# Performance work log

Measured on AMD Instinct MI355X. Metric: run time of the kernel, lower is better.

The kernel has to match this reference:

```python
import jax, jax.numpy as jnp
import numpy as np

# hyperparams matching init_kwargs
T_LEN = 1024
T_LATENCY = 7
TB = T_LATENCY + 1          # t_len_block
N_OUT = 1024
BATCH = 32
FS_SCALE = 10.0             # FastSigmoid default scale


@jax.custom_vjp
def fast_sigmoid(x):
    # forward: Heaviside; backward: fast-sigmoid surrogate
    return (x > 0).astype(x.dtype)

def _fs_fwd(x):
    return (x > 0).astype(x.dtype), x

def _fs_bwd(x, g):
    return (g / (FS_SCALE * jnp.abs(x) + 1.0) ** 2,)

fast_sigmoid.defvjp(_fs_fwd, _fs_bwd)


def setup_inputs() -> dict:
    key = jax.random.key(0)
    k1, k2, k3, k4 = jax.random.split(key, 4)
    x = jax.random.normal(k1, (T_LEN, BATCH, N_OUT), dtype=jnp.float32) * 0.6
    # raw params; forward applies the clamp/abs 'properties' of the module
    beta_raw = jax.random.uniform(k2, (N_OUT,), minval=0.7, maxval=0.99, dtype=jnp.float32)
    p_raw = jax.random.uniform(k3, (N_OUT,), minval=0.5, maxval=0.95, dtype=jnp.float32)
    b_raw = jax.random.uniform(k4, (N_OUT,), minval=0.2, maxval=1.0, dtype=jnp.float32)
    return {"x": x, "beta_raw": beta_raw, "p_raw": p_raw, "b_raw": b_raw}


def reference(x, beta_raw, p_raw, b_raw):
    T, B, N = x.shape
    tb = TB
    n_blocks = T // tb  # t_pad == 0 by construction
    dt = x.dtype

    # clamped properties
    beta = jnp.clip(beta_raw, 0.001, 0.999)          # [N]
    p = jnp.clip(jnp.abs(p_raw), 0.0, 0.999)         # [N]
    bb = jnp.clip(jnp.abs(b_raw), 0.001, 1.0)        # [N]

    t_idx = jnp.arange(tb)
    expo = t_idx[:, None] - t_idx[None, :]            # [tb,tb], t - s
    lower = expo >= 0
    # causal decay kernel: beta^(t-s) for s<=t  (grouped conv1d equivalent)
    beta_pow = jnp.where(lower[:, :, None],
                         beta[None, None, :] ** jnp.maximum(expo, 0)[:, :, None].astype(dt),
                         jnp.zeros((), dt))           # [tb,tb,N]
    # phi kernel: weight (t-s+1) for s<=t  (conv2d equivalent)
    phi = jnp.where(lower, (expo + 1).astype(dt), jnp.zeros((), dt))  # [tb,tb]
    p_exp = jnp.arange(1, tb + 1, dtype=dt)           # [tb]
    p_pow = p[None, :] ** p_exp[:, None]              # [tb,N]
    inv_p = 1.0 / p                                   # [N]

    def body(carry, x_slice):
        spikes, z, int_mem, a_kernel = carry          # [tb,B,N],[tb,B,N],[B,N],[tb,B,N]
        sg = jax.lax.stop_gradient(spikes)            # detach_spike_grad=True
        maskf = (jnp.max(sg, axis=0) > 0).astype(dt)  # [B,N] any spike in prev block
        # refractory masking of input
        xs = jnp.where(z < maskf[None], jnp.zeros((), dt), x_slice)
        v_init = int_mem * (1.0 - maskf)
        # adaptation update
        a_at_spike = jnp.sum(a_kernel * sg, axis=0) + inv_p          # [B,N]
        decay_steps = jnp.sum(z > 1, axis=0).astype(dt)              # [B,N]
        new_a = a_at_spike * jnp.power(p[None, :], decay_steps)
        a = a_kernel[-1] * (1.0 - maskf) + new_a * maskf             # [B,N]
        a_k = p_pow[:, None, :] * a[None]                             # [tb,B,N]
        v_th = 1.0 + bb[None, None, :] * a_k                          # [tb,B,N]
        # --- Block forward ---
        cur = xs.at[0].add(beta[None, :] * v_init)
        membrane = jnp.einsum('tsn,sbn->tbn', beta_pow, cur)          # causal decayed sum
        faulty = fast_sigmoid(membrane - v_th)                        # [tb,B,N] 0/1
        z_new = jnp.einsum('ts,sbn->tbn', phi, faulty)
        # g(): keep only entries exactly 1, straight-through grad
        spikes_new = z_new - jax.lax.stop_gradient(
            jnp.where(z_new == 1.0, jnp.zeros((), dt), z_new))
        return (spikes_new, z_new, membrane[-1], a_k), spikes_new

    z0 = jnp.zeros((tb, B, N), dt)
    carry0 = (z0, z0, jnp.zeros((B, N), dt), z0)
    xb = x.reshape(n_blocks, tb, B, N)
    _, out = jax.lax.scan(body, carry0, xb)
    return out.reshape(T, B, N)
```

## Files before the change

kernel.cpp:

```cpp
#include <hip/hip_runtime.h>


constexpr int T_LEN = 1024;
constexpr int TB    = 8;
constexpr int NBLK  = T_LEN / TB;
constexpr int BATCH = 32;
constexpr int NOUT  = 1024;
constexpr int BN    = BATCH * NOUT;
constexpr int PF    = 16;

typedef float f4 __attribute__((ext_vector_type(4)));

#define WAITVM_T(N, A, B) \
    asm volatile("s_waitcnt vmcnt(" #N ")" : "+v"(A), "+v"(B) :: "memory")

#define GLOAD(DST, ADDR) \
    asm volatile("global_load_dwordx4 %0, %1, off" \
                 : "=v"(DST) : "v"(ADDR) : "memory")

__global__ __launch_bounds__(64, 1)
void snn_blocks_kernel(const float* __restrict__ x,
                       const float* __restrict__ beta_raw,
                       const float* __restrict__ p_raw,
                       const float* __restrict__ b_raw,
                       float* __restrict__ out)
{
    __shared__ float inbuf[TB][64];
    __shared__ float sbuf[TB][64];

    const int lane = threadIdx.x;
    const int wg0  = blockIdx.x * 64;
    const int gid  = wg0 + lane;
    const int n    = gid & (NOUT - 1);

    const int rowoff = lane >> 4;
    const int coloff = wg0 + (lane & 15) * 4;

    double beta = (double)beta_raw[n];
    beta = beta < 0.001 ? 0.001 : (beta > 0.999 ? 0.999 : beta);
    double p = fabs((double)p_raw[n]);
    p = p > 0.999 ? 0.999 : p;
    double bb = fabs((double)b_raw[n]);
    bb = bb < 0.001 ? 0.001 : (bb > 1.0 ? 1.0 : bb);
    const double inv_p = 1.0 / p;

    double ppow[9];
    ppow[0] = 1.0;
#pragma unroll
    for (int i = 1; i <= 8; ++i) ppow[i] = ppow[i - 1] * p;

    double bbp[8];
#pragma unroll
    for (int t = 0; t < 8; ++t) bbp[t] = bb * ppow[t + 1];

    double m = 0.0;
    double a = 0.0;
    int    maskf = 0;
    int    decay = 0;
    double ssum  = 0.0;
    int    zzero = 0xFF;

    f4 fr[PF][2];

#pragma unroll
    for (int k = 0; k < PF; ++k) {
        GLOAD(fr[k][0], x + (ptrdiff_t)(k * TB + rowoff) * BN + coloff);
        GLOAD(fr[k][1], x + (ptrdiff_t)(k * TB + 4 + rowoff) * BN + coloff);
    }

    auto body = [&](int blk, f4 v0, f4 v1) {
        *(f4*)&inbuf[rowoff][(lane & 15) * 4]     = v0;
        *(f4*)&inbuf[rowoff + 4][(lane & 15) * 4] = v1;
        float cur[8];
#pragma unroll
        for (int t = 0; t < 8; ++t) cur[t] = inbuf[t][lane];

        const double a_at = a * ssum + inv_p;
        double pd = 1.0;
        pd *= (decay & 1) ? p       : 1.0;
        pd *= (decay & 2) ? ppow[2] : 1.0;
        pd *= (decay & 4) ? ppow[4] : 1.0;
        pd *= (decay & 8) ? ppow[8] : 1.0;
        const double new_a = a_at * pd;

        if (maskf) { a = new_a;     m = 0.0; }
        else       { a = ppow[8] * a;        }

        int nmaskf = 0, ndecay = 0, nzzero = 0;
        double nssum = 0.0;
        int c = 0, zc = 0;
#pragma unroll
        for (int t = 0; t < 8; ++t) {
            double xv = (double)cur[t];
            if (maskf && ((zzero >> t) & 1)) xv = 0.0;
            m = beta * m + xv;
            const double vth = 1.0 + bbp[t] * a;
            const int f = (m - vth > 0.0) ? 1 : 0;
            c  += f;
            zc += c;
            nmaskf |= (zc == 1);
            ndecay += (zc > 1) ? 1 : 0;
            nssum  += (zc == 1) ? ppow[t + 1] : 0.0;
            nzzero |= (zc == 0) ? (1 << t) : 0;
            sbuf[t][lane] = (zc == 1) ? 1.0f : 0.0f;
        }
        maskf = nmaskf; decay = ndecay; ssum = nssum; zzero = nzzero;

        const float* sflat = &sbuf[0][0];
        f4 s0 = *(const f4*)(sflat + lane * 4);
        f4 s1 = *(const f4*)(sflat + 256 + lane * 4);
        __builtin_nontemporal_store(
            s0, (f4*)(out + (ptrdiff_t)(blk * TB + rowoff) * BN + coloff));
        __builtin_nontemporal_store(
            s1, (f4*)(out + (ptrdiff_t)(blk * TB + 4 + rowoff) * BN + coloff));
    };

#define STEP(N, BLK, SL) do {                                              \
        WAITVM_T(N, fr[SL][0], fr[SL][1]);                                 \
        body((BLK), fr[SL][0], fr[SL][1]);                                 \
        const int pfb = (BLK) + PF;                                        \
        GLOAD(fr[SL][0], x + (ptrdiff_t)(pfb * TB + rowoff) * BN + coloff);\
        GLOAD(fr[SL][1], x + (ptrdiff_t)(pfb * TB + 4 + rowoff) * BN + coloff);\
    } while (0)

#define STEPT(N, BLK, SL) do {                                             \
        WAITVM_T(N, fr[SL][0], fr[SL][1]);                                 \
        body((BLK), fr[SL][0], fr[SL][1]);                                 \
    } while (0)

#pragma unroll
    for (int j = 0; j < 16; ++j) STEP(30, j, j);

#pragma unroll 1
    for (int r = 1; r < 7; ++r) {
#pragma unroll
        for (int i = 0; i < 16; ++i) STEP(60, r * 16 + i, i);
    }

#pragma unroll
    for (int k = 0; k < 16; ++k) STEPT(30, 112 + k, k);
}

extern "C" void kernel_launch(void* const* d_in, const int* in_sizes, int n_in,
                              void* d_out, int out_size, void* d_ws, size_t ws_size,
                              hipStream_t stream) {
    const float* x        = (const float*)d_in[0];
    const float* beta_raw = (const float*)d_in[1];
    const float* p_raw    = (const float*)d_in[2];
    const float* b_raw    = (const float*)d_in[3];
    float* out            = (float*)d_out;

    dim3 grid(BN / 64);
    dim3 block(64);
    snn_blocks_kernel<<<grid, block, 0, stream>>>(x, beta_raw, p_raw, b_raw, out);
}
```

Before: 250.9 us.

## Replace inline-asm prefetch ring with compiler-scheduled loads and halve prefetch depth

Drops the hand-written global_load/s_waitcnt inline assembly and uses plain vector loads, leaving the compiler to insert waitcnts, with sched_barrier fences between block steps. The prefetch ring shrinks from 16 to 8 blocks and the loop becomes uniform, with a guard on the tail prefetch. Fewer loads stay in flight, which may expose more memory latency in this latency-bound single-wave-per-block kernel. In exchange it frees registers and may let the compiler place waits more precisely.

```diff
diff --git a/kernel.cpp b/kernel.cpp
--- a/kernel.cpp
+++ b/kernel.cpp
@@ -7,16 +7,9 @@
 constexpr int BATCH = 32;
 constexpr int NOUT  = 1024;
 constexpr int BN    = BATCH * NOUT;
-constexpr int PF    = 16;
+constexpr int PF    = 8;
 
 typedef float f4 __attribute__((ext_vector_type(4)));
-
-#define WAITVM_T(N, A, B) \
-    asm volatile("s_waitcnt vmcnt(" #N ")" : "+v"(A), "+v"(B) :: "memory")
-
-#define GLOAD(DST, ADDR) \
-    asm volatile("global_load_dwordx4 %0, %1, off" \
-                 : "=v"(DST) : "v"(ADDR) : "memory")
 
 __global__ __launch_bounds__(64, 1)
 void snn_blocks_kernel(const float* __restrict__ x,
@@ -62,10 +55,12 @@
 
     f4 fr[PF][2];
 
+    const float* xbase = x + (ptrdiff_t)rowoff * BN + coloff;
+
 #pragma unroll
     for (int k = 0; k < PF; ++k) {
-        GLOAD(fr[k][0], x + (ptrdiff_t)(k * TB + rowoff) * BN + coloff);
-        GLOAD(fr[k][1], x + (ptrdiff_t)(k * TB + 4 + rowoff) * BN + coloff);
+        fr[k][0] = *(const f4*)(xbase + (ptrdiff_t)(k * TB) * BN);
+        fr[k][1] = *(const f4*)(xbase + (ptrdiff_t)(k * TB + 4) * BN);
     }
 
     auto body = [&](int blk, f4 v0, f4 v1) {
@@ -115,30 +110,20 @@
             s1, (f4*)(out + (ptrdiff_t)(blk * TB + 4 + rowoff) * BN + coloff));
     };
 
-#define STEP(N, BLK, SL) do {                                              \
-        WAITVM_T(N, fr[SL][0], fr[SL][1]);                                 \
-        body((BLK), fr[SL][0], fr[SL][1]);                                 \
-        const int pfb = (BLK) + PF;                                        \
-        GLOAD(fr[SL][0], x + (ptrdiff_t)(pfb * TB + rowoff) * BN + coloff);\
-        GLOAD(fr[SL][1], x + (ptrdiff_t)(pfb * TB + 4 + rowoff) * BN + coloff);\
-    } while (0)
-
-#define STEPT(N, BLK, SL) do {                                             \
-        WAITVM_T(N, fr[SL][0], fr[SL][1]);                                 \
-        body((BLK), fr[SL][0], fr[SL][1]);                                 \
-    } while (0)
-
+#pragma unroll 1
+    for (int r = 0; r < NBLK / PF; ++r) {
 #pragma unroll
-    for (int j = 0; j < 16; ++j) STEP(30, j, j);
-
-#pragma unroll 1
-    for (int r = 1; r < 7; ++r) {
-#pragma unroll
-        for (int i = 0; i < 16; ++i) STEP(60, r * 16 + i, i);
+        for (int i = 0; i < PF; ++i) {
+            const int blk = r * PF + i;
+            body(blk, fr[i][0], fr[i][1]);
+            const int pfb = blk + PF;
+            if (pfb < NBLK) {
+                fr[i][0] = *(const f4*)(xbase + (ptrdiff_t)(pfb * TB) * BN);
+                fr[i][1] = *(const f4*)(xbase + (ptrdiff_t)(pfb * TB + 4) * BN);
+            }
+            __builtin_amdgcn_sched_barrier(0);
+        }
     }
-
-#pragma unroll
-    for (int k = 0; k < 16; ++k) STEPT(30, 112 + k, k);
 }
 
 extern "C" void kernel_launch(void* const* d_in, const int* in_sizes, int n_in,
```

Result: faster. 244.2 us (-2.7%).
